# Kernel optimization log

Hardware: AMD Instinct MI355X
Metric: run time of the kernel (lower is better)

The kernel has to match this reference:

```python
import math
import jax, jax.numpy as jnp
import numpy as np

B, T, E, H = 2, 2048, 1024, 16
HS = E // H  # head size = 64
NEG = jnp.float32(-1e10)


def setup_inputs() -> dict:
    key = jax.random.key(0)
    ks = jax.random.split(key, 7)
    return {
        "query": jax.random.normal(ks[0], (B, T, E), jnp.float32),
        "key": jax.random.normal(ks[1], (B, T, E), jnp.float32),
        "value": jax.random.normal(ks[2], (B, T, E), jnp.float32),
        "Wq": jax.random.normal(ks[3], (E, E), jnp.float32) * 0.02,
        "Wk": jax.random.normal(ks[4], (E, E), jnp.float32) * 0.02,
        "Wv": jax.random.normal(ks[5], (E, E), jnp.float32) * 0.02,
        "Wp": jax.random.normal(ks[6], (E, E), jnp.float32) * 0.02,
    }


def reference(query, key, value, Wq, Wk, Wv, Wp):
    # QKV projections (no bias), split into heads: [B, H, T, HS]
    q = (query @ Wq).reshape(B, T, H, HS).transpose(0, 2, 1, 3)
    k = (key @ Wk).reshape(B, T, H, HS).transpose(0, 2, 1, 3)
    v = (value @ Wv).reshape(B, T, H, HS).transpose(0, 2, 1, 3)
    # scaled dot-product scores [B, H, T, T]
    att = jnp.einsum("bhqd,bhkd->bhqk", q, k) / math.sqrt(HS)
    # additive causal mask (tril allowed)
    causal = jnp.tril(jnp.ones((T, T), dtype=att.dtype))
    att = att + jnp.where(causal == 0, NEG, jnp.float32(0.0))[None, None]
    att = jax.nn.softmax(att, axis=-1)
    # dropout rate 0 / deterministic -> identity
    y = jnp.einsum("bhqk,bhkd->bhqd", att, v)
    y = y.transpose(0, 2, 1, 3).reshape(B, T, E)
    y = y @ Wp
    return y
```

## Files before the change

kernel.cpp:

```cpp
#include <hip/hip_runtime.h>

#define TB 2
#define TT 2048
#define TE 1024
#define TH 16
#define THS 64
#define TM (TB * TT)

typedef __attribute__((ext_vector_type(8))) short short8;
typedef __attribute__((ext_vector_type(4))) float f32x4;
typedef __attribute__((ext_vector_type(16))) float f32x16;

__device__ __forceinline__ f32x4 mfma16(short8 a, short8 b, f32x4 c) {
    return __builtin_amdgcn_mfma_f32_16x16x32_bf16(a, b, c, 0, 0, 0);
}
__device__ __forceinline__ f32x16 mfma32(short8 a, short8 b, f32x16 c) {
    return __builtin_amdgcn_mfma_f32_32x32x16_bf16(a, b, c, 0, 0, 0);
}

__device__ __forceinline__ void gload_lds16(const void* g, void* l) {
    __builtin_amdgcn_global_load_lds(
        (const __attribute__((address_space(1))) void*)g,
        (__attribute__((address_space(3))) void*)l, 16, 0, 0);
}

__device__ __forceinline__ unsigned short f2bf(float f) {
    unsigned int u = __float_as_uint(f);
    u += 0x7fff + ((u >> 16) & 1);
    return (unsigned short)(u >> 16);
}

__device__ __forceinline__ unsigned cvtpk_bf16(float lo, float hi) {
    unsigned r;
    asm("v_cvt_pk_bf16_f32 %0, %1, %2" : "=v"(r) : "v"(lo), "v"(hi));
    return r;
}
__device__ __forceinline__ void plswap(unsigned& a, unsigned& b) {
    asm("v_permlane32_swap_b32 %0, %1" : "+v"(a), "+v"(b));
}

__global__ __launch_bounds__(256) void prep(
    const float* __restrict__ q, const float* __restrict__ k,
    const float* __restrict__ v, unsigned short* __restrict__ qc,
    unsigned short* __restrict__ kc, unsigned short* __restrict__ vc,
    const float* __restrict__ W0, const float* __restrict__ W1,
    const float* __restrict__ W2, const float* __restrict__ W3,
    unsigned short* __restrict__ T0, unsigned short* __restrict__ T1,
    unsigned short* __restrict__ T2, unsigned short* __restrict__ T3) {
    __shared__ float Ts[32][33];
    const int y = blockIdx.y;
    if (y < 3) {
        const float* src = (y == 0) ? q : (y == 1) ? k : v;
        unsigned short* dst = (y == 0) ? qc : (y == 1) ? kc : vc;
        const int i = blockIdx.x * 256 + threadIdx.x;
        float4 vv = ((const float4*)src)[i];
        ushort4 o;
        o.x = f2bf(vv.x); o.y = f2bf(vv.y); o.z = f2bf(vv.z); o.w = f2bf(vv.w);
        ((ushort4*)dst)[i] = o;
    } else {
        const int x = blockIdx.x;
        const int z = x >> 10, rem = x & 1023;
        const float* W = (z == 0) ? W0 : (z == 1) ? W1 : (z == 2) ? W2 : W3;
        unsigned short* Wt = (z == 0) ? T0 : (z == 1) ? T1 : (z == 2) ? T2 : T3;
        const int r0 = ((rem >> 5) & 31) * 32, c0 = (rem & 31) * 32;
        const int t = threadIdx.x;
        const int r = t >> 3, c = (t & 7) * 4;
        float4 vv = *(const float4*)&W[(size_t)(r0 + r) * TE + c0 + c];
        Ts[r][c] = vv.x; Ts[r][c + 1] = vv.y; Ts[r][c + 2] = vv.z; Ts[r][c + 3] = vv.w;
        __syncthreads();
        ushort4 o;
        o.x = f2bf(Ts[c + 0][r]); o.y = f2bf(Ts[c + 1][r]);
        o.z = f2bf(Ts[c + 2][r]); o.w = f2bf(Ts[c + 3][r]);
        *(ushort4*)&Wt[(size_t)(c0 + r) * TE + r0 + c] = o;
    }
}

__global__ __launch_bounds__(256, 2) void gemm_qkv(
    const unsigned short* __restrict__ qc, const unsigned short* __restrict__ kc,
    const unsigned short* __restrict__ vc, const unsigned short* __restrict__ Wqt,
    const unsigned short* __restrict__ Wkt, const unsigned short* __restrict__ Wvt,
    unsigned short* __restrict__ Qb, unsigned short* __restrict__ Kb,
    unsigned short* __restrict__ Vt) {
    __shared__ unsigned short LDS[32768];

    const int lin = blockIdx.x;
    const int swz = (lin & 7) * 96 + (lin >> 3);
    const int z = swz >> 8;
    const int rem = swz & 255;
    const int bm = (rem & 31) * 128, bn = (rem >> 5) * 128;

    const unsigned short* A  = (z == 0) ? qc : (z == 1) ? kc : vc;
    const unsigned short* Bt = (z == 0) ? Wqt : (z == 1) ? Wkt : Wvt;

    const int tid = threadIdx.x;
    const int w = tid >> 6, lane = tid & 63;
    const int quad = lane >> 4, l16 = lane & 15;
    const int wm = (w >> 1) * 64, wn = (w & 1) * 64;

    const int srow = lane >> 2;
    const int scol = (((lane & 3) ^ ((srow >> 1) & 3))) * 8;
    const int rchunk = (quad ^ ((l16 >> 1) & 3)) * 8;

    f32x4 acc[4][4];
    const f32x4 fz = {0.f, 0.f, 0.f, 0.f};
    #pragma unroll
    for (int i = 0; i < 4; ++i)
        #pragma unroll
        for (int j = 0; j < 4; ++j) acc[i][j] = fz;

    auto stageA = [&](int t, int half) {
        const int buf = t & 1, k0 = t * 64;
        #pragma unroll
        for (int j = 0; j < 2; ++j) {
            const int e = w * 2 + j;
            const int kk = e >> 2, i2 = e & 3;
            const int cr = half * 2 + (i2 & 1) + ((i2 >> 1) << 2);
            gload_lds16(A + (size_t)(bm + cr * 16 + srow) * TE + k0 + kk * 32 + scol,
                        &LDS[buf * 8192 + kk * 4096 + cr * 512 + lane * 8]);
        }
    };
    auto stageB = [&](int t, int half) {
        const int buf = t & 1, k0 = t * 64;
        #pragma unroll
        for (int j = 0; j < 2; ++j) {
            const int e = w * 2 + j;
            const int kk = e >> 2, i2 = e & 3;
            const int cc = half * 2 + (i2 & 1) + ((i2 >> 1) << 2);
            gload_lds16(Bt + (size_t)(bn + cc * 16 + srow) * TE + k0 + kk * 32 + scol,
                        &LDS[16384 + buf * 8192 + kk * 4096 + cc * 512 + lane * 8]);
        }
    };

    auto ktile = [&](int t, bool st, bool last) {
        const int buf = t & 1;
        const unsigned short* Al = &LDS[buf * 8192];
        const unsigned short* Bl = &LDS[16384 + buf * 8192];
        short8 af[2][2], blo[2][2], bhi[2][2];
        #pragma unroll
        for (int mi = 0; mi < 2; ++mi)
            #pragma unroll
            for (int kk = 0; kk < 2; ++kk)
                af[mi][kk] = *(const short8*)&Al[kk * 4096 + ((w >> 1) * 4 + mi) * 512 + l16 * 32 + rchunk];
        #pragma unroll
        for (int nj = 0; nj < 2; ++nj)
            #pragma unroll
            for (int kk = 0; kk < 2; ++kk)
                blo[nj][kk] = *(const short8*)&Bl[kk * 4096 + ((w & 1) * 4 + nj) * 512 + l16 * 32 + rchunk];
        asm volatile("s_waitcnt lgkmcnt(0)" ::: "memory");
        __builtin_amdgcn_sched_barrier(0);
        __builtin_amdgcn_s_setprio(1);
        #pragma unroll
        for (int mi = 0; mi < 2; ++mi)
            #pragma unroll
            for (int nj = 0; nj < 2; ++nj)
                #pragma unroll
                for (int kk = 0; kk < 2; ++kk)
                    acc[mi][nj] = mfma16(af[mi][kk], blo[nj][kk], acc[mi][nj]);
        __builtin_amdgcn_s_setprio(0);
        __builtin_amdgcn_sched_barrier(0);
        __builtin_amdgcn_s_barrier();
        #pragma unroll
        for (int nj = 0; nj < 2; ++nj)
            #pragma unroll
            for (int kk = 0; kk < 2; ++kk)
                bhi[nj][kk] = *(const short8*)&Bl[kk * 4096 + ((w & 1) * 4 + 2 + nj) * 512 + l16 * 32 + rchunk];
        if (st) { stageA(t + 2, 0); stageB(t + 2, 0); }
        asm volatile("s_waitcnt lgkmcnt(0)" ::: "memory");
        __builtin_amdgcn_sched_barrier(0);
        __builtin_amdgcn_s_setprio(1);
        #pragma unroll
        for (int mi = 0; mi < 2; ++mi)
            #pragma unroll
            for (int nj = 0; nj < 2; ++nj)
                #pragma unroll
                for (int kk = 0; kk < 2; ++kk)
                    acc[mi][2 + nj] = mfma16(af[mi][kk], bhi[nj][kk], acc[mi][2 + nj]);
        __builtin_amdgcn_s_setprio(0);
        __builtin_amdgcn_sched_barrier(0);
        __builtin_amdgcn_s_barrier();
        #pragma unroll
        for (int mi = 0; mi < 2; ++mi)
            #pragma unroll
            for (int kk = 0; kk < 2; ++kk)
                af[mi][kk] = *(const short8*)&Al[kk * 4096 + ((w >> 1) * 4 + 2 + mi) * 512 + l16 * 32 + rchunk];
        if (st) stageB(t + 2, 1);
        asm volatile("s_waitcnt lgkmcnt(0)" ::: "memory");
        __builtin_amdgcn_sched_barrier(0);
        __builtin_amdgcn_s_setprio(1);
        #pragma unroll
        for (int mi = 0; mi < 2; ++mi)
            #pragma unroll
            for (int nj = 0; nj < 2; ++nj)
                #pragma unroll
                for (int kk = 0; kk < 2; ++kk)
                    acc[2 + mi][nj] = mfma16(af[mi][kk], blo[nj][kk], acc[2 + mi][nj]);
        __builtin_amdgcn_s_setprio(0);
        __builtin_amdgcn_sched_barrier(0);
        __builtin_amdgcn_s_barrier();
        if (st) stageA(t + 2, 1);
        __builtin_amdgcn_s_setprio(1);
        #pragma unroll
        for (int mi = 0; mi < 2; ++mi)
            #pragma unroll
            for (int nj = 0; nj < 2; ++nj)
                #pragma unroll
                for (int kk = 0; kk < 2; ++kk)
                    acc[2 + mi][2 + nj] = mfma16(af[mi][kk], bhi[nj][kk], acc[2 + mi][2 + nj]);
        __builtin_amdgcn_s_setprio(0);
        __builtin_amdgcn_sched_barrier(0);
        if (st) {
            asm volatile("s_waitcnt vmcnt(8)" ::: "memory");
        } else if (last) {
            asm volatile("s_waitcnt vmcnt(0)" ::: "memory");
        }
        __builtin_amdgcn_s_barrier();
    };

    stageA(0, 0); stageB(0, 0); stageB(0, 1); stageA(0, 1);
    stageA(1, 0); stageB(1, 0); stageB(1, 1); stageA(1, 1);
    asm volatile("s_waitcnt vmcnt(8)" ::: "memory");
    __builtin_amdgcn_s_barrier();

    #pragma unroll 1
    for (int t = 0; t < 14; ++t) ktile(t, true, false);
    ktile(14, false, true);
    ktile(15, false, false);

    if (z < 2) {
        unsigned short* Cb = (z == 0) ? Qb : Kb;
        const float sc = (z == 0) ? 0.18033688011112042f : 1.0f;
        #pragma unroll
        for (int mi = 0; mi < 4; ++mi)
            #pragma unroll
            for (int nj = 0; nj < 4; ++nj) {
                const int m0 = bm + wm + mi * 16 + quad * 4;
                const int n = bn + wn + nj * 16 + l16;
                #pragma unroll
                for (int r = 0; r < 4; ++r)
                    Cb[(size_t)(m0 + r) * TE + n] = f2bf(acc[mi][nj][r] * sc);
            }
    } else {
        #pragma unroll
        for (int mi = 0; mi < 4; ++mi)
            #pragma unroll
            for (int nj = 0; nj < 4; ++nj) {
                const int m0 = bm + wm + mi * 16 + quad * 4;
                const int n = bn + wn + nj * 16 + l16;
                ushort4 o;
                o.x = f2bf(acc[mi][nj][0]); o.y = f2bf(acc[mi][nj][1]);
                o.z = f2bf(acc[mi][nj][2]); o.w = f2bf(acc[mi][nj][3]);
                size_t idx = ((size_t)((m0 >> 11) * TH + (n >> 6)) * THS + (n & 63)) * TT + (m0 & (TT - 1));
                *(ushort4*)&Vt[idx] = o;
            }
    }
}

__global__ __launch_bounds__(256, 2) void gemm_out(
    const unsigned short* __restrict__ A, const unsigned short* __restrict__ Bt,
    float* __restrict__ C) {
    __shared__ unsigned short As[2][128 * 32];
    __shared__ unsigned short Bs[2][64 * 32];

    const int tid = threadIdx.x;
    const int w = tid >> 6, lane = tid & 63;
    const int quad = lane >> 4, l16 = lane & 15;
    const int bm = blockIdx.x * 128, bn = blockIdx.y * 64;
    const int wm = (w >> 1) * 64, wn = (w & 1) * 32;

    f32x4 acc[4][2];
    const f32x4 fz = {0.f, 0.f, 0.f, 0.f};
    #pragma unroll
    for (int i = 0; i < 4; ++i)
        #pragma unroll
        for (int j = 0; j < 2; ++j) acc[i][j] = fz;

    const int srow = lane >> 2;
    const int scol = (((lane & 3) ^ ((srow >> 1) & 3))) * 8;
    const int rchunk = (quad ^ ((l16 >> 1) & 3)) * 8;

    auto stage = [&](int k0, int buf) {
        #pragma unroll
        for (int i = 0; i < 3; ++i) {
            const int ch = w * 3 + i;
            if (ch < 8)
                gload_lds16(A + (size_t)(bm + ch * 16 + srow) * TE + k0 + scol,
                            &As[buf][ch * 512 + lane * 8]);
            else
                gload_lds16(Bt + (size_t)(bn + (ch - 8) * 16 + srow) * TE + k0 + scol,
                            &Bs[buf][(ch - 8) * 512 + lane * 8]);
        }
    };

    stage(0, 0);
    int cur = 0;
    for (int k0 = 0; k0 < TE; k0 += 32) {
        __syncthreads();
        if (k0 + 32 < TE) stage(k0 + 32, cur ^ 1);

        short8 af[4], bf[2];
        #pragma unroll
        for (int i = 0; i < 4; ++i)
            af[i] = *(const short8*)&As[cur][(wm + i * 16 + l16) * 32 + rchunk];
        #pragma unroll
        for (int j = 0; j < 2; ++j)
            bf[j] = *(const short8*)&Bs[cur][(wn + j * 16 + l16) * 32 + rchunk];
        #pragma unroll
        for (int i = 0; i < 4; ++i)
            #pragma unroll
            for (int j = 0; j < 2; ++j)
                acc[i][j] = mfma16(af[i], bf[j], acc[i][j]);
        cur ^= 1;
    }

    #pragma unroll
    for (int i = 0; i < 4; ++i)
        #pragma unroll
        for (int j = 0; j < 2; ++j) {
            const int m0 = bm + wm + i * 16 + quad * 4;
            const int n = bn + wn + j * 16 + l16;
            #pragma unroll
            for (int r = 0; r < 4; ++r)
                C[(size_t)(m0 + r) * TE + n] = acc[i][j][r];
        }
}

__global__ __launch_bounds__(256, 2) void attn_mfma(
    const unsigned short* __restrict__ Q, const unsigned short* __restrict__ K,
    const unsigned short* __restrict__ Vt, unsigned short* __restrict__ O) {
    __shared__ unsigned short S[32768];

    const int tid = threadIdx.x;
    const int lane = tid & 63;
    const int wl = tid >> 6;
    const int rl = lane & 31, x = lane >> 5;

    const int lin = blockIdx.x;
    const int bh = lin & 31;
    const int it = 15 - (lin >> 5);
    const int b = bh >> 4, h = bh & 15;
    const int nt = it + 1;

    const unsigned short* Kg = K + (size_t)b * TT * TE + h * THS;
    const unsigned short* Vg = Vt + (size_t)bh * THS * TT;

    short8 aq[4];
    {
        const size_t rQ = (size_t)(b * TT + it * 128 + wl * 32 + rl) * TE + h * THS + x * 8;
        #pragma unroll
        for (int c = 0; c < 4; ++c) aq[c] = *(const short8*)&Q[rQ + c * 16];
    }

    const int srow = lane >> 2;
    const int scol = (((lane & 3) ^ ((srow >> 1) & 3))) * 8;

    auto stage = [&](int p, int buf) {
        const int sub = wl >> 1;
        const int k0 = (2 * p + sub) * 64;
        if ((wl & 1) == 0) {
            #pragma unroll
            for (int ee = 0; ee < 8; ++ee) {
                const int kk = ee >> 2, r16 = (ee & 3) * 16;
                gload_lds16(Kg + (size_t)(k0 + r16 + srow) * TE + kk * 32 + scol,
                            &S[buf * 16384 + sub * 4096 + ee * 512 + lane * 8]);
            }
        } else {
            #pragma unroll
            for (int ee = 0; ee < 8; ++ee) {
                const int kk = ee >> 2, r16 = (ee & 3) * 16;
                gload_lds16(Vg + (size_t)(r16 + srow) * TT + k0 + kk * 32 + scol,
                            &S[buf * 16384 + 8192 + sub * 4096 + ee * 512 + lane * 8]);
            }
        }
    };

    stage(0, 0);

    const int xr = (rl >> 1) & 3;
    const int q0 = it * 128;
    const int qv = q0 + wl * 32 + rl;
    const int qwMin = q0 + wl * 32;
    const int qwMax = qwMin + 31;

    f32x16 accO0, accO1, fz16;
    #pragma unroll
    for (int i = 0; i < 16; ++i) { accO0[i] = 0.f; accO1[i] = 0.f; fz16[i] = 0.f; }
    float lacc = 0.f;

    #pragma unroll 1
    for (int i = 0; i < nt; ++i) {
        const int buf = i & 1;
        asm volatile("s_waitcnt vmcnt(0)" ::: "memory");
        __builtin_amdgcn_s_barrier();
        __builtin_amdgcn_sched_barrier(0);
        if (i + 1 < nt) stage(i + 1, buf ^ 1);

        #pragma unroll
        for (int sub = 0; sub < 2; ++sub) {
            const int k0 = (2 * i + sub) * 64;
            if (k0 > qwMax) continue;

            const unsigned short* Kb = &S[buf * 16384 + sub * 4096];
            const unsigned short* Vb = &S[buf * 16384 + 8192 + sub * 4096];

            f32x16 sa0 = fz16, sa1 = fz16;
            #pragma unroll
            for (int c = 0; c < 4; ++c) {
                const int off = (c >> 1) * 2048 + ((((c & 1) * 2 + x) ^ xr)) * 8;
                short8 kf0 = *(const short8*)&Kb[off + rl * 32];
                short8 kf1 = *(const short8*)&Kb[off + (32 + rl) * 32];
                sa0 = mfma32(kf0, aq[c], sa0);
                sa1 = mfma32(kf1, aq[c], sa1);
            }

            const bool open = (k0 + 63 <= qwMin);
            short8 pb[4];
            float lp0 = 0.f, lp1 = 0.f, lp2 = 0.f, lp3 = 0.f;
            #pragma unroll
            for (int mt = 0; mt < 2; ++mt) {
                float pv[16];
                #pragma unroll
                for (int r = 0; r < 16; ++r) {
                    const float sv = (mt == 0) ? sa0[r] : sa1[r];
                    float e = __builtin_amdgcn_exp2f(sv);
                    if (!open) {
                        const int kg = k0 + mt * 32 + (r & 3) + 8 * (r >> 2) + 4 * x;
                        e = (kg > qv) ? 0.f : e;
                    }
                    pv[r] = e;
                    if ((r & 3) == 0) lp0 += e;
                    else if ((r & 3) == 1) lp1 += e;
                    else if ((r & 3) == 2) lp2 += e;
                    else lp3 += e;
                }
                unsigned w0 = cvtpk_bf16(pv[0], pv[1]),   w1 = cvtpk_bf16(pv[2], pv[3]);
                unsigned w2 = cvtpk_bf16(pv[4], pv[5]),   w3 = cvtpk_bf16(pv[6], pv[7]);
                unsigned w4 = cvtpk_bf16(pv[8], pv[9]),   w5 = cvtpk_bf16(pv[10], pv[11]);
                unsigned w6 = cvtpk_bf16(pv[12], pv[13]), w7 = cvtpk_bf16(pv[14], pv[15]);
                plswap(w0, w2); plswap(w1, w3);
                plswap(w4, w6); plswap(w5, w7);
                union { unsigned u[4]; short8 s8; } f0, f1;
                f0.u[0] = w0; f0.u[1] = w1; f0.u[2] = w2; f0.u[3] = w3;
                f1.u[0] = w4; f1.u[1] = w5; f1.u[2] = w6; f1.u[3] = w7;
                pb[mt * 2] = f0.s8; pb[mt * 2 + 1] = f1.s8;
            }
            lacc += (lp0 + lp1) + (lp2 + lp3);

            __builtin_amdgcn_s_setprio(1);
            #pragma unroll
            for (int c = 0; c < 4; ++c) {
                const int off = (c >> 1) * 2048 + ((((c & 1) * 2 + x) ^ xr)) * 8;
                short8 vf0 = *(const short8*)&Vb[off + rl * 32];
                short8 vf1 = *(const short8*)&Vb[off + (32 + rl) * 32];
                accO0 = mfma32(vf0, pb[c], accO0);
                accO1 = mfma32(vf1, pb[c], accO1);
            }
            __builtin_amdgcn_s_setprio(0);
        }
    }

    lacc += __shfl_xor(lacc, 32);
    const float linv = 1.0f / lacc;

    unsigned short* Og = O + (size_t)(b * TT + q0 + wl * 32 + rl) * TE + h * THS;
    #pragma unroll
    for (int dt = 0; dt < 2; ++dt)
        #pragma unroll
        for (int q4 = 0; q4 < 4; ++q4) {
            float o0, o1, o2, o3;
            if (dt == 0) { o0 = accO0[q4*4+0]; o1 = accO0[q4*4+1]; o2 = accO0[q4*4+2]; o3 = accO0[q4*4+3]; }
            else         { o0 = accO1[q4*4+0]; o1 = accO1[q4*4+1]; o2 = accO1[q4*4+2]; o3 = accO1[q4*4+3]; }
            const int dbase = 8 * q4 + 4 * x + 32 * dt;
            ushort4 o;
            o.x = f2bf(o0 * linv); o.y = f2bf(o1 * linv);
            o.z = f2bf(o2 * linv); o.w = f2bf(o3 * linv);
            *(ushort4*)&Og[dbase] = o;
        }
}

extern "C" void kernel_launch(void* const* d_in, const int* in_sizes, int n_in,
                              void* d_out, int out_size, void* d_ws, size_t ws_size,
                              hipStream_t stream) {
    const float* q  = (const float*)d_in[0];
    const float* k  = (const float*)d_in[1];
    const float* v  = (const float*)d_in[2];
    const float* Wq = (const float*)d_in[3];
    const float* Wk = (const float*)d_in[4];
    const float* Wv = (const float*)d_in[5];
    const float* Wp = (const float*)d_in[6];
    float* out = (float*)d_out;

    const size_t se = (size_t)TM * TE;
    unsigned short* qc  = (unsigned short*)d_ws;
    unsigned short* kc  = qc + se;
    unsigned short* vc  = kc + se;
    unsigned short* Qb  = vc + se;
    unsigned short* Kb  = Qb + se;
    unsigned short* Vt  = Kb + se;
    unsigned short* Ob  = Vt + se;
    unsigned short* Wqt = Ob + se;
    unsigned short* Wkt = Wqt + (size_t)TE * TE;
    unsigned short* Wvt = Wkt + (size_t)TE * TE;
    unsigned short* Wpt = Wvt + (size_t)TE * TE;

    prep<<<dim3(4096, 4), 256, 0, stream>>>(q, k, v, qc, kc, vc,
                                            Wq, Wk, Wv, Wp, Wqt, Wkt, Wvt, Wpt);

    gemm_qkv<<<768, 256, 0, stream>>>(qc, kc, vc, Wqt, Wkt, Wvt, Qb, Kb, Vt);

    attn_mfma<<<512, 256, 0, stream>>>(Qb, Kb, Vt, Ob);

    gemm_out<<<dim3(TM / 128, TE / 64), 256, 0, stream>>>(Ob, Wpt, out);
}
```

Before: 207.8 us.

## Store K/V in fragment-ready tiled layout and load attention operands directly to registers

The QKV projection epilogue now writes K and V into a per-head, per-64-key tiled layout that matches the MFMA operand fragments. The attention kernel drops its shared-memory staging, barriers and async LDS loads, and instead reads K and V fragments straight from global memory into registers, with K for the next tile prefetched in a double-buffered register scheme. Each wave also runs only the key tiles its own query rows need, rather than the block-level count. This removes LDS traffic and block-wide synchronisation, but each wave now reads K/V from global or L2 on its own with no sharing across waves, and register pressure goes up. The scattered scalar K stores in the epilogue may also cost more.

Result: faster. 193.6 us (-6.9%).

```diff
diff --git a/kernel.cpp b/kernel.cpp
--- a/kernel.cpp
+++ b/kernel.cpp
@@ -226,9 +226,8 @@
     ktile(14, false, true);
     ktile(15, false, false);
 
-    if (z < 2) {
-        unsigned short* Cb = (z == 0) ? Qb : Kb;
-        const float sc = (z == 0) ? 0.18033688011112042f : 1.0f;
+    if (z == 0) {
+        const float sc = 0.18033688011112042f;
         #pragma unroll
         for (int mi = 0; mi < 4; ++mi)
             #pragma unroll
@@ -237,20 +236,42 @@
                 const int n = bn + wn + nj * 16 + l16;
                 #pragma unroll
                 for (int r = 0; r < 4; ++r)
-                    Cb[(size_t)(m0 + r) * TE + n] = f2bf(acc[mi][nj][r] * sc);
+                    Qb[(size_t)(m0 + r) * TE + n] = f2bf(acc[mi][nj][r] * sc);
             }
-    } else {
+    } else if (z == 1) {
         #pragma unroll
         for (int mi = 0; mi < 4; ++mi)
             #pragma unroll
             for (int nj = 0; nj < 4; ++nj) {
                 const int m0 = bm + wm + mi * 16 + quad * 4;
                 const int n = bn + wn + nj * 16 + l16;
+                const int hh = n >> 6, dd = n & 63;
+                const int dpart = (dd >> 4) * 512 + ((dd >> 3) & 1) * 8 + (dd & 7);
+                #pragma unroll
+                for (int r = 0; r < 4; ++r) {
+                    const int m = m0 + r;
+                    const int t = m & (TT - 1), bb = m >> 11;
+                    const size_t addr = ((size_t)((bb * TH + hh) * 32 + (t >> 6))) * 4096
+                                      + ((t >> 5) & 1) * 2048 + dpart + (t & 31) * 16;
+                    Kb[addr] = f2bf(acc[mi][nj][r]);
+                }
+            }
+    } else {
+        #pragma unroll
+        for (int mi = 0; mi < 4; ++mi)
+            #pragma unroll
+            for (int nj = 0; nj < 4; ++nj) {
+                const int m0 = bm + wm + mi * 16 + quad * 4;
+                const int n = bn + wn + nj * 16 + l16;
+                const int hh = n >> 6, dd = n & 63;
+                const int t0 = m0 & (TT - 1), bb = m0 >> 11;
+                const size_t addr = ((size_t)((bb * TH + hh) * 32 + (t0 >> 6))) * 4096
+                                  + (dd >> 5) * 2048 + ((t0 & 63) >> 4) * 512
+                                  + (dd & 31) * 16 + ((t0 >> 3) & 1) * 8 + (t0 & 7);
                 ushort4 o;
                 o.x = f2bf(acc[mi][nj][0]); o.y = f2bf(acc[mi][nj][1]);
                 o.z = f2bf(acc[mi][nj][2]); o.w = f2bf(acc[mi][nj][3]);
-                size_t idx = ((size_t)((m0 >> 11) * TH + (n >> 6)) * THS + (n & 63)) * TT + (m0 & (TT - 1));
-                *(ushort4*)&Vt[idx] = o;
+                *(ushort4*)&Vt[addr] = o;
             }
     }
 }
@@ -325,10 +346,8 @@
 }
 
 __global__ __launch_bounds__(256, 2) void attn_mfma(
-    const unsigned short* __restrict__ Q, const unsigned short* __restrict__ K,
-    const unsigned short* __restrict__ Vt, unsigned short* __restrict__ O) {
-    __shared__ unsigned short S[32768];
-
+    const unsigned short* __restrict__ Q, const unsigned short* __restrict__ Kf,
+    const unsigned short* __restrict__ Vf, unsigned short* __restrict__ O) {
     const int tid = threadIdx.x;
     const int lane = tid & 63;
     const int wl = tid >> 6;
@@ -338,130 +357,106 @@
     const int bh = lin & 31;
     const int it = 15 - (lin >> 5);
     const int b = bh >> 4, h = bh & 15;
-    const int nt = it + 1;
-
-    const unsigned short* Kg = K + (size_t)b * TT * TE + h * THS;
-    const unsigned short* Vg = Vt + (size_t)bh * THS * TT;
+
+    const int qs = it * 128 + wl * 32;
+    const int qv = qs + rl;
+    const int nt = ((qs + 31) >> 6) + 1;
 
     short8 aq[4];
     {
-        const size_t rQ = (size_t)(b * TT + it * 128 + wl * 32 + rl) * TE + h * THS + x * 8;
+        const size_t rQ = (size_t)(b * TT + qs + rl) * TE + h * THS + x * 8;
         #pragma unroll
         for (int c = 0; c < 4; ++c) aq[c] = *(const short8*)&Q[rQ + c * 16];
     }
 
-    const int srow = lane >> 2;
-    const int scol = (((lane & 3) ^ ((srow >> 1) & 3))) * 8;
-
-    auto stage = [&](int p, int buf) {
-        const int sub = wl >> 1;
-        const int k0 = (2 * p + sub) * 64;
-        if ((wl & 1) == 0) {
-            #pragma unroll
-            for (int ee = 0; ee < 8; ++ee) {
-                const int kk = ee >> 2, r16 = (ee & 3) * 16;
-                gload_lds16(Kg + (size_t)(k0 + r16 + srow) * TE + kk * 32 + scol,
-                            &S[buf * 16384 + sub * 4096 + ee * 512 + lane * 8]);
-            }
-        } else {
-            #pragma unroll
-            for (int ee = 0; ee < 8; ++ee) {
-                const int kk = ee >> 2, r16 = (ee & 3) * 16;
-                gload_lds16(Vg + (size_t)(r16 + srow) * TT + k0 + kk * 32 + scol,
-                            &S[buf * 16384 + 8192 + sub * 4096 + ee * 512 + lane * 8]);
-            }
-        }
-    };
-
-    stage(0, 0);
-
-    const int xr = (rl >> 1) & 3;
-    const int q0 = it * 128;
-    const int qv = q0 + wl * 32 + rl;
-    const int qwMin = q0 + wl * 32;
-    const int qwMax = qwMin + 31;
+    const unsigned short* Kt = Kf + (size_t)bh * 32 * 4096;
+    const unsigned short* Vb = Vf + (size_t)bh * 32 * 4096;
+    const int loff = rl * 16 + x * 8;
+
+    auto loadK = [&](int j, short8* d) {
+        const unsigned short* base = Kt + j * 4096 + loff;
+        #pragma unroll
+        for (int f = 0; f < 8; ++f)
+            d[f] = *(const short8*)&base[(f >> 2) * 2048 + (f & 3) * 512];
+    };
+    auto loadV = [&](int j, short8* d) {
+        const unsigned short* base = Vb + j * 4096 + loff;
+        #pragma unroll
+        for (int f = 0; f < 8; ++f)
+            d[f] = *(const short8*)&base[(f >> 2) * 2048 + (f & 3) * 512];
+    };
 
     f32x16 accO0, accO1, fz16;
     #pragma unroll
     for (int i = 0; i < 16; ++i) { accO0[i] = 0.f; accO1[i] = 0.f; fz16[i] = 0.f; }
     float lacc = 0.f;
 
+    auto compute = [&](int j, const short8* kf, const short8* vf) {
+        const int k0 = j * 64;
+        f32x16 sa0 = fz16, sa1 = fz16;
+        #pragma unroll
+        for (int c = 0; c < 4; ++c) {
+            sa0 = mfma32(kf[c], aq[c], sa0);
+            sa1 = mfma32(kf[4 + c], aq[c], sa1);
+        }
+        const bool open = (j < nt - 1);
+        short8 pb[4];
+        float lp0 = 0.f, lp1 = 0.f, lp2 = 0.f, lp3 = 0.f;
+        #pragma unroll
+        for (int mt = 0; mt < 2; ++mt) {
+            float pv[16];
+            #pragma unroll
+            for (int r = 0; r < 16; ++r) {
+                const float sv = (mt == 0) ? sa0[r] : sa1[r];
+                float e = __builtin_amdgcn_exp2f(sv);
+                if (!open) {
+                    const int kg = k0 + mt * 32 + (r & 3) + 8 * (r >> 2) + 4 * x;
+                    e = (kg > qv) ? 0.f : e;
+                }
+                pv[r] = e;
+                if ((r & 3) == 0) lp0 += e;
+                else if ((r & 3) == 1) lp1 += e;
+                else if ((r & 3) == 2) lp2 += e;
+                else lp3 += e;
+            }
+            unsigned w0 = cvtpk_bf16(pv[0], pv[1]),   w1 = cvtpk_bf16(pv[2], pv[3]);
+            unsigned w2 = cvtpk_bf16(pv[4], pv[5]),   w3 = cvtpk_bf16(pv[6], pv[7]);
+            unsigned w4 = cvtpk_bf16(pv[8], pv[9]),   w5 = cvtpk_bf16(pv[10], pv[11]);
+            unsigned w6 = cvtpk_bf16(pv[12], pv[13]), w7 = cvtpk_bf16(pv[14], pv[15]);
+            plswap(w0, w2); plswap(w1, w3);
+            plswap(w4, w6); plswap(w5, w7);
+            union { unsigned u[4]; short8 s8; } f0, f1;
+            f0.u[0] = w0; f0.u[1] = w1; f0.u[2] = w2; f0.u[3] = w3;
+            f1.u[0] = w4; f1.u[1] = w5; f1.u[2] = w6; f1.u[3] = w7;
+            pb[mt * 2] = f0.s8; pb[mt * 2 + 1] = f1.s8;
+        }
+        lacc += (lp0 + lp1) + (lp2 + lp3);
+        #pragma unroll
+        for (int c = 0; c < 4; ++c) {
+            accO0 = mfma32(vf[c], pb[c], accO0);
+            accO1 = mfma32(vf[4 + c], pb[c], accO1);
+        }
+    };
+
+    short8 ka[8], kb[8], va[8];
+    loadK(0, ka);
+    int j = 0;
     #pragma unroll 1
-    for (int i = 0; i < nt; ++i) {
-        const int buf = i & 1;
-        asm volatile("s_waitcnt vmcnt(0)" ::: "memory");
-        __builtin_amdgcn_s_barrier();
-        __builtin_amdgcn_sched_barrier(0);
-        if (i + 1 < nt) stage(i + 1, buf ^ 1);
-
-        #pragma unroll
-        for (int sub = 0; sub < 2; ++sub) {
-            const int k0 = (2 * i + sub) * 64;
-            if (k0 > qwMax) continue;
-
-            const unsigned short* Kb = &S[buf * 16384 + sub * 4096];
-            const unsigned short* Vb = &S[buf * 16384 + 8192 + sub * 4096];
-
-            f32x16 sa0 = fz16, sa1 = fz16;
-            #pragma unroll
-            for (int c = 0; c < 4; ++c) {
-                const int off = (c >> 1) * 2048 + ((((c & 1) * 2 + x) ^ xr)) * 8;
-                short8 kf0 = *(const short8*)&Kb[off + rl * 32];
-                short8 kf1 = *(const short8*)&Kb[off + (32 + rl) * 32];
-                sa0 = mfma32(kf0, aq[c], sa0);
-                sa1 = mfma32(kf1, aq[c], sa1);
-            }
-
-            const bool open = (k0 + 63 <= qwMin);
-            short8 pb[4];
-            float lp0 = 0.f, lp1 = 0.f, lp2 = 0.f, lp3 = 0.f;
-            #pragma unroll
-            for (int mt = 0; mt < 2; ++mt) {
-                float pv[16];
-                #pragma unroll
-                for (int r = 0; r < 16; ++r) {
-                    const float sv = (mt == 0) ? sa0[r] : sa1[r];
-                    float e = __builtin_amdgcn_exp2f(sv);
-                    if (!open) {
-                        const int kg = k0 + mt * 32 + (r & 3) + 8 * (r >> 2) + 4 * x;
-                        e = (kg > qv) ? 0.f : e;
-                    }
-                    pv[r] = e;
-                    if ((r & 3) == 0) lp0 += e;
-                    else if ((r & 3) == 1) lp1 += e;
-                    else if ((r & 3) == 2) lp2 += e;
-                    else lp3 += e;
-                }
-                unsigned w0 = cvtpk_bf16(pv[0], pv[1]),   w1 = cvtpk_bf16(pv[2], pv[3]);
-                unsigned w2 = cvtpk_bf16(pv[4], pv[5]),   w3 = cvtpk_bf16(pv[6], pv[7]);
-                unsigned w4 = cvtpk_bf16(pv[8], pv[9]),   w5 = cvtpk_bf16(pv[10], pv[11]);
-                unsigned w6 = cvtpk_bf16(pv[12], pv[13]), w7 = cvtpk_bf16(pv[14], pv[15]);
-                plswap(w0, w2); plswap(w1, w3);
-                plswap(w4, w6); plswap(w5, w7);
-                union { unsigned u[4]; short8 s8; } f0, f1;
-                f0.u[0] = w0; f0.u[1] = w1; f0.u[2] = w2; f0.u[3] = w3;
-                f1.u[0] = w4; f1.u[1] = w5; f1.u[2] = w6; f1.u[3] = w7;
-                pb[mt * 2] = f0.s8; pb[mt * 2 + 1] = f1.s8;
-            }
-            lacc += (lp0 + lp1) + (lp2 + lp3);
-
-            __builtin_amdgcn_s_setprio(1);
-            #pragma unroll
-            for (int c = 0; c < 4; ++c) {
-                const int off = (c >> 1) * 2048 + ((((c & 1) * 2 + x) ^ xr)) * 8;
-                short8 vf0 = *(const short8*)&Vb[off + rl * 32];
-                short8 vf1 = *(const short8*)&Vb[off + (32 + rl) * 32];
-                accO0 = mfma32(vf0, pb[c], accO0);
-                accO1 = mfma32(vf1, pb[c], accO1);
-            }
-            __builtin_amdgcn_s_setprio(0);
-        }
+    while (true) {
+        loadV(j, va);
+        if (j + 1 < nt) loadK(j + 1, kb);
+        compute(j, ka, va);
+        ++j; if (j >= nt) break;
+        loadV(j, va);
+        if (j + 1 < nt) loadK(j + 1, ka);
+        compute(j, kb, va);
+        ++j; if (j >= nt) break;
     }
 
     lacc += __shfl_xor(lacc, 32);
     const float linv = 1.0f / lacc;
 
-    unsigned short* Og = O + (size_t)(b * TT + q0 + wl * 32 + rl) * TE + h * THS;
+    unsigned short* Og = O + (size_t)(b * TT + qs + rl) * TE + h * THS;
     #pragma unroll
     for (int dt = 0; dt < 2; ++dt)
         #pragma unroll
```
